# Performance work log

Measured on AMD Instinct MI355X. Metric: run time of the kernel, lower is better.

Reference implementation:

```python
import jax, jax.numpy as jnp
import numpy as np
from jax import lax

D_MODEL = 1024
D_STATE = 128
D_CONV = 4
EXPAND = 2
N_HEADS = 32
CHUNK = 64
D_INNER = EXPAND * D_MODEL                 # 2048
CONV_DIM = D_INNER + 2 * D_STATE           # 2304
D_IN_PROJ = 2 * D_INNER + 2 * D_STATE + N_HEADS  # 4384
HEAD_DIM = D_INNER // N_HEADS              # 64
EPS = 1e-5


def setup_inputs() -> dict:
    key = jax.random.key(0)
    ks = jax.random.split(key, 10)
    u = jax.random.normal(ks[0], (4, 4096, D_MODEL), dtype=jnp.float32)
    in_proj_w = jax.random.normal(ks[1], (D_IN_PROJ, D_MODEL), dtype=jnp.float32) * 0.02
    conv_w = jax.random.normal(ks[2], (CONV_DIM, 1, D_CONV), dtype=jnp.float32) * 0.3
    conv_b = jnp.zeros((CONV_DIM,), dtype=jnp.float32)
    dt_bias = jax.random.uniform(ks[3], (N_HEADS,), minval=-0.5, maxval=0.5, dtype=jnp.float32)
    A_log = jax.random.uniform(ks[4], (N_HEADS,), minval=-0.1, maxval=-0.01, dtype=jnp.float32)
    D = jax.random.uniform(ks[5], (N_HEADS,), minval=0.9, maxval=1.1, dtype=jnp.float32)
    norm_w = jnp.ones((D_INNER,), dtype=jnp.float32)
    out_proj_w = jax.random.normal(ks[6], (D_MODEL, D_INNER), dtype=jnp.float32) * 0.02
    return {"u": u, "in_proj_w": in_proj_w, "conv_w": conv_w, "conv_b": conv_b,
            "dt_bias": dt_bias, "A_log": A_log, "D": D, "norm_w": norm_w,
            "out_proj_w": out_proj_w}


def segsum(x):
    """Stable segment sum. x: (..., T) -> (..., T, T); exp of it is 1-semiseparable."""
    T = x.shape[-1]
    xe = jnp.broadcast_to(x[..., :, None], x.shape + (T,))  # '... d -> ... d e'
    mask_strict = jnp.tril(jnp.ones((T, T), dtype=bool), k=-1)
    xe = jnp.where(mask_strict, xe, 0.0)
    seg = jnp.cumsum(xe, axis=-2)
    mask_incl = jnp.tril(jnp.ones((T, T), dtype=bool), k=0)
    return jnp.where(mask_incl, seg, -jnp.inf)


def ssd(x, A, B, C):
    """x:(b,L,h,p)  A:(b,L,h)  B,C:(b,L,h,n). L multiple of CHUNK."""
    b, Lp, h, p = x.shape
    n = B.shape[-1]
    c = Lp // CHUNK
    x = x.reshape(b, c, CHUNK, h, p)
    A = A.reshape(b, c, CHUNK, h).transpose(0, 3, 1, 2)       # (b,h,c,l)
    B = B.reshape(b, c, CHUNK, h, n)
    C = C.reshape(b, c, CHUNK, h, n)
    A_cumsum = jnp.cumsum(A, axis=-1)                          # (b,h,c,l)
    L = jnp.exp(segsum(A))                                     # (b,h,c,l,l)
    # intra-chunk (diagonal blocks)
    Y_diag = jnp.einsum('bclhn,bcshn,bhcls,bcshp->bclhp', C, B, L, x)
    # chunk-final states
    decay_states = jnp.exp(A_cumsum[:, :, :, -1:] - A_cumsum)  # (b,h,c,l)
    states = jnp.einsum('bclhn,bhcl,bclhp->bchpn', B, decay_states, x)
    init = jnp.zeros_like(states[:, :1])
    states = jnp.concatenate([init, states], axis=1)           # (b,c+1,h,p,n)
    decay_chunk = jnp.exp(segsum(jnp.pad(A_cumsum[:, :, :, -1], ((0, 0), (0, 0), (1, 0)))))
    new_states = jnp.einsum('bhzc,bchpn->bzhpn', decay_chunk, states)
    states, final_state = new_states[:, :-1], new_states[:, -1]
    # inter-chunk (off-diagonal) contribution
    state_decay_out = jnp.exp(A_cumsum)
    Y_off = jnp.einsum('bclhn,bchpn,bhcl->bclhp', C, states, state_decay_out)
    Y = (Y_diag + Y_off).reshape(b, Lp, h, p)
    return Y, final_state


def _forward(u, in_proj_w, conv_w, conv_b, dt_bias, A_log, D, norm_w, out_proj_w):
    b, seq_len, _ = u.shape
    pad = CHUNK - seq_len % CHUNK  # note: full extra chunk when seq_len % CHUNK == 0 (faithful)
    u = jnp.pad(u, ((0, 0), (0, pad), (0, 0)))
    Lp = u.shape[1]
    A = -jnp.exp(A_log)                                        # (h,)
    zxbcdt = jnp.einsum('bld,ed->ble', u, in_proj_w)           # (b,Lp,D_IN_PROJ)
    z = zxbcdt[..., :D_INNER]
    xBC = zxbcdt[..., D_INNER:D_INNER + CONV_DIM]
    dt = zxbcdt[..., -N_HEADS:]
    # causal depthwise conv1d + silu
    xc = xBC.transpose(0, 2, 1)                                # (b,conv_dim,Lp)
    xc = lax.conv_general_dilated(xc, conv_w, window_strides=(1,),
                                  padding=[(D_CONV - 1, 0)],
                                  feature_group_count=CONV_DIM,
                                  dimension_numbers=('NCH', 'OIH', 'NCH'))
    xBC = jax.nn.silu((xc + conv_b[None, :, None]).transpose(0, 2, 1))
    x = xBC[..., :D_INNER].reshape(b, Lp, N_HEADS, HEAD_DIM)
    Bm = xBC[..., D_INNER:D_INNER + D_STATE]
    Cm = xBC[..., D_INNER + D_STATE:]
    Bm = jnp.broadcast_to(Bm[:, :, None, :], (b, Lp, N_HEADS, D_STATE))
    Cm = jnp.broadcast_to(Cm[:, :, None, :], (b, Lp, N_HEADS, D_STATE))
    dt = jax.nn.softplus(dt + dt_bias)                         # (b,Lp,h)
    y, _ = ssd(x * dt[..., None], A * dt, Bm, Cm)
    y = y + x * D[None, None, :, None]
    y = y.reshape(b, Lp, D_INNER)
    # gated RMSNorm
    t = y * jax.nn.silu(z)
    t = t * jax.lax.rsqrt(jnp.mean(t * t, axis=-1, keepdims=True) + EPS) * norm_w
    out = jnp.einsum('bld,ed->ble', t, out_proj_w)
    return out[:, :seq_len]


def reference(u, in_proj_w, conv_w, conv_b, dt_bias, A_log, D, norm_w, out_proj_w):
    return _forward(u, in_proj_w, conv_w, conv_b, dt_bias, A_log, D, norm_w, out_proj_w)
```

## Files before the change

### kernel.cpp

```cpp
#include <hip/hip_runtime.h>
#include <hip/hip_bf16.h>
#include <math.h>


#define BL    16384
#define NCONV 2304
#define LDXP  2336

typedef __hip_bfloat16 bf16;
typedef __attribute__((ext_vector_type(8))) short bf16x8_i;
typedef __attribute__((ext_vector_type(4))) float f32x4;

union BF8 { uint4 u; bf16 h[8]; };
union BF2 { uint u; bf16 h[2]; };

__device__ __forceinline__ void gload_lds16(const void* g, void* l) {
  __builtin_amdgcn_global_load_lds(
      (__attribute__((address_space(1))) void*)(uintptr_t)g,
      (__attribute__((address_space(3))) void*)(uint32_t)(uintptr_t)l,
      16, 0, 0);
}

template<typename TC, bool CLAMPB>
__global__ __launch_bounds__(256) void gemm_bt_mfma(
    const bf16* __restrict__ A, int lda,
    const bf16* __restrict__ B, int ldb,
    TC* __restrict__ C, int ldc, int N, int K)
{
  __shared__ __align__(16) bf16 As[128 * 32];
  __shared__ __align__(16) bf16 Bs[128 * 32];
  const int tid  = threadIdx.x;
  const int lane = tid & 63;
  const int wid  = tid >> 6;

  const int gx  = gridDim.x;
  const int nwg = gx * gridDim.y;
  const int q   = nwg >> 3;
  int id = blockIdx.y * gx + blockIdx.x;
  id = (id & 7) * q + (id >> 3);
  const int bm = (id / gx) * 128;
  const int bn = (id % gx) * 128;

  const int wr = (wid >> 1) * 64;
  const int wc = (wid & 1) * 64;

  f32x4 acc[4][4] = {};

  int aoff[4], boff[4];
  #pragma unroll
  for (int i = 0; i < 4; ++i) {
    aoff[i] = (wr + i * 16 + (lane & 15)) * 32 + (lane >> 4) * 8;
    boff[i] = (wc + i * 16 + (lane & 15)) * 32 + (lane >> 4) * 8;
  }

  const int srow = tid >> 2, scol = (tid & 3) * 8;
  int brow0 = bn + srow, brow1 = bn + 64 + srow;
  if (CLAMPB) { brow0 = min(brow0, N - 1); brow1 = min(brow1, N - 1); }
  const bf16* pA0 = A + (size_t)(bm + srow) * lda + scol;
  const bf16* pA1 = pA0 + (size_t)lda * 64;
  const bf16* pB0 = B + (size_t)brow0 * ldb + scol;
  const bf16* pB1 = B + (size_t)brow1 * ldb + scol;
  bf16* lA0 = As + wid * 512;
  bf16* lA1 = As + 2048 + wid * 512;
  bf16* lB0 = Bs + wid * 512;
  bf16* lB1 = Bs + 2048 + wid * 512;

  for (int k0 = 0; k0 < K; k0 += 32) {
    gload_lds16(pA0, lA0);
    gload_lds16(pA1, lA1);
    gload_lds16(pB0, lB0);
    gload_lds16(pB1, lB1);
    pA0 += 32; pA1 += 32; pB0 += 32; pB1 += 32;
    __syncthreads();
    bf16x8_i af[4], bfr[4];
    #pragma unroll
    for (int i = 0; i < 4; ++i) {
      af[i]  = *(const bf16x8_i*)(As + aoff[i]);
      bfr[i] = *(const bf16x8_i*)(Bs + boff[i]);
    }
    #pragma unroll
    for (int i = 0; i < 4; ++i)
      #pragma unroll
      for (int j = 0; j < 4; ++j)
        acc[i][j] = __builtin_amdgcn_mfma_f32_16x16x32_bf16(
            af[i], bfr[j], acc[i][j], 0, 0, 0);
    __syncthreads();
  }

  const int cr = (lane >> 4) * 4;
  const int cc = lane & 15;
  #pragma unroll
  for (int i = 0; i < 4; ++i) {
    #pragma unroll
    for (int j = 0; j < 4; ++j) {
      const int n = bn + wc + j * 16 + cc;
      if (n < N) {
        #pragma unroll
        for (int r = 0; r < 4; ++r) {
          const int m = bm + wr + i * 16 + cr + r;
          if constexpr (sizeof(TC) == 2)
            ((bf16*)C)[(size_t)m * ldc + n] = __float2bfloat16(acc[i][j][r]);
          else
            ((float*)C)[(size_t)m * ldc + n] = acc[i][j][r];
        }
      }
    }
  }
}

__global__ __launch_bounds__(256) void cvt_f32_bf16(
    const float* __restrict__ in, bf16* __restrict__ out)
{
  const size_t i = (size_t)(blockIdx.x * 256 + threadIdx.x) * 8;
  float4 a = *(const float4*)(in + i);
  float4 b = *(const float4*)(in + i + 4);
  BF8 o;
  o.h[0] = __float2bfloat16(a.x); o.h[1] = __float2bfloat16(a.y);
  o.h[2] = __float2bfloat16(a.z); o.h[3] = __float2bfloat16(a.w);
  o.h[4] = __float2bfloat16(b.x); o.h[5] = __float2bfloat16(b.y);
  o.h[6] = __float2bfloat16(b.z); o.h[7] = __float2bfloat16(b.w);
  *(uint4*)(out + i) = o.u;
}

__global__ __launch_bounds__(256) void dtsp_atot_kernel(
    const bf16* __restrict__ xpre, const float* __restrict__ dt_bias,
    const float* __restrict__ A_log,
    float* __restrict__ dtT, float* __restrict__ Atot)
{
  const int c = blockIdx.x, b = blockIdx.y;
  const int tid = threadIdx.x;
  const int h = tid & 31, lg = tid >> 5;
  __shared__ float red[8][33];
  float s = 0.f, vals[8];
  const bf16* src = xpre + ((size_t)b * 4096 + c * 64 + lg * 8) * LDXP + 2304 + h;
  const float bias = dt_bias[h];
  #pragma unroll
  for (int k = 0; k < 8; ++k) {
    float v = __bfloat162float(src[(size_t)k * LDXP]) + bias;
    v = fmaxf(v, 0.f) + log1pf(expf(-fabsf(v)));
    vals[k] = v; s += v;
  }
  float* dp = dtT + ((size_t)(b * 32 + h)) * 4096 + c * 64 + lg * 8;
  #pragma unroll
  for (int k = 0; k < 8; ++k) dp[k] = vals[k];
  red[lg][h] = s;
  __syncthreads();
  if (tid < 32) {
    float t = 0.f;
    #pragma unroll
    for (int g = 0; g < 8; ++g) t += red[g][tid];
    Atot[((size_t)b * 64 + c) * 32 + tid] = -expf(A_log[tid]) * t;
  }
}

__global__ __launch_bounds__(256) void conv_silu_kernel(
    const bf16* __restrict__ xpre,
    const float* __restrict__ conv_w,
    const float* __restrict__ conv_b,
    bf16* __restrict__ xBC)
{
  const int ch = blockIdx.x * 256 + threadIdx.x;
  const int t0 = blockIdx.y * 8;
  const int bb = blockIdx.z;
  const float w0 = conv_w[ch*4+0], w1 = conv_w[ch*4+1];
  const float w2 = conv_w[ch*4+2], w3 = conv_w[ch*4+3];
  const float bias = conv_b[ch];
  const size_t rb = (size_t)bb * 4096;
  const bf16* src = xpre + ch;
  float v0 = (t0 >= 3) ? __bfloat162float(src[(rb + t0 - 3) * LDXP]) : 0.f;
  float v1 = (t0 >= 2) ? __bfloat162float(src[(rb + t0 - 2) * LDXP]) : 0.f;
  float v2 = (t0 >= 1) ? __bfloat162float(src[(rb + t0 - 1) * LDXP]) : 0.f;
  for (int t = t0; t < t0 + 8; ++t) {
    float v3 = __bfloat162float(src[(rb + t) * LDXP]);
    float o = bias + w0*v0 + w1*v1 + w2*v2 + w3*v3;
    o = o / (1.f + expf(-o));
    xBC[(rb + t) * NCONV + ch] = __float2bfloat16(o);
    v0 = v1; v1 = v2; v2 = v3;
  }
}

__device__ __forceinline__ int swz8(int row) { return ((row >> 3) & 7) << 3; }

__global__ __launch_bounds__(256) void s1_localstate(
    const bf16* __restrict__ xBC, const float* __restrict__ dtT,
    const float* __restrict__ A_log, bf16* __restrict__ states, int b)
{
  const int hh = blockIdx.x, c = blockIdx.y;
  const int tid = threadIdx.x, lane = tid & 63, wid = tid >> 6;
  __shared__ bf16 BT[128 * 72];
  __shared__ bf16 xwT[64 * 72];
  __shared__ bf16 Sout[64 * 136];
  const size_t r0 = (size_t)b * 4096 + (size_t)c * 64;

  BF8 regB[4], regx[2];
  #pragma unroll
  for (int k = 0; k < 4; ++k) {
    int id = tid + k * 256, l = id >> 4, n0 = (id & 15) * 8;
    regB[k].u = *(const uint4*)(xBC + (r0 + l) * NCONV + 2048 + n0);
  }
  #pragma unroll
  for (int k = 0; k < 2; ++k) {
    int id = tid + k * 256, l = id >> 3, p0 = (id & 7) * 8;
    regx[k].u = *(const uint4*)(xBC + (r0 + l) * NCONV + hh * 64 + p0);
  }

  float d = dtT[((size_t)(b * 32 + hh)) * 4096 + c * 64 + lane];
  float Ah = -expf(A_log[hh]);
  float v = Ah * d;
  #pragma unroll
  for (int off = 1; off < 64; off <<= 1) {
    float up = __shfl_up(v, off, 64);
    if (lane >= off) v += up;
  }
  const float At = __shfl(v, 63, 64);
  const float w = d * __expf(At - v);

  #pragma unroll
  for (int k = 0; k < 4; ++k) {
    int id = tid + k * 256, l = id >> 4, n0 = (id & 15) * 8;
    #pragma unroll
    for (int j = 0; j < 8; ++j) {
      int n = n0 + j;
      BT[n * 72 + (l ^ swz8(n))] = regB[k].h[j];
    }
  }
  #pragma unroll
  for (int k = 0; k < 2; ++k) {
    int id = tid + k * 256, l = id >> 3, p0 = (id & 7) * 8;
    float wv = __shfl(w, l, 64);
    #pragma unroll
    for (int j = 0; j < 8; ++j) {
      int p = p0 + j;
      xwT[p * 72 + (l ^ swz8(p))] =
          __float2bfloat16(__bfloat162float(regx[k].h[j]) * wv);
    }
  }
  __syncthreads();

  const int wr = (wid & 1) * 32;
  const int wc = (wid >> 1) * 64;
  f32x4 acc[2][4] = {};
  #pragma unroll
  for (int ks = 0; ks < 2; ++ks) {
    const int k0 = ks * 32 + (lane >> 4) * 8;
    bf16x8_i a[2], bb[4];
    #pragma unroll
    for (int i = 0; i < 2; ++i) {
      int p = wr + i * 16 + (lane & 15);
      a[i] = *(const bf16x8_i*)(xwT + p * 72 + (k0 ^ swz8(p)));
    }
    #pragma unroll
    for (int j = 0; j < 4; ++j) {
      int n = wc + j * 16 + (lane & 15);
      bb[j] = *(const bf16x8_i*)(BT + n * 72 + (k0 ^ swz8(n)));
    }
    #pragma unroll
    for (int i = 0; i < 2; ++i)
      #pragma unroll
      for (int j = 0; j < 4; ++j)
        acc[i][j] = __builtin_amdgcn_mfma_f32_16x16x32_bf16(
            a[i], bb[j], acc[i][j], 0, 0, 0);
  }

  const int cr = (lane >> 4) * 4, cn = lane & 15;
  #pragma unroll
  for (int i = 0; i < 2; ++i)
    #pragma unroll
    for (int j = 0; j < 4; ++j)
      #pragma unroll
      for (int r = 0; r < 4; ++r)
        Sout[(wr + i * 16 + cr + r) * 136 + (wc + j * 16 + cn)] =
            __float2bfloat16(acc[i][j][r]);
  __syncthreads();
  bf16* sb = states + ((size_t)c * 32 + hh) * 8192;
  #pragma unroll
  for (int k = 0; k < 4; ++k) {
    int id = tid + k * 256, p = id >> 4, n0 = (id & 15) * 8;
    *(uint4*)(sb + p * 128 + n0) = *(const uint4*)(Sout + p * 136 + n0);
  }
}

__global__ __launch_bounds__(256) void s2_scan(
    bf16* __restrict__ states, const float* __restrict__ Atot, int b)
{
  const int h  = blockIdx.x >> 4;
  const int p  = ((blockIdx.x & 15) << 2) | (threadIdx.x >> 6);
  const int n0 = (threadIdx.x & 63) * 2;
  __shared__ float ec[64];
  if (threadIdx.x < 64)
    ec[threadIdx.x] = expf(Atot[((size_t)b * 64 + threadIdx.x) * 32 + h]);
  __syncthreads();
  bf16* ptr = states + ((size_t)h * 64 + p) * 128 + n0;
  const size_t cs = (size_t)32 * 8192;
  float ca = 0.f, cb = 0.f;
  BF2 g0, g1, g2, g3, q0, q1, q2, q3;
  g0.u = *(const uint*)(ptr + 0 * cs);
  g1.u = *(const uint*)(ptr + 1 * cs);
  g2.u = *(const uint*)(ptr + 2 * cs);
  g3.u = *(const uint*)(ptr + 3 * cs);
  for (int g = 0; g < 16; ++g) {
    const int c0 = g * 4;
    if (g < 15) {
      q0.u = *(const uint*)(ptr + (c0 + 4) * cs);
      q1.u = *(const uint*)(ptr + (c0 + 5) * cs);
      q2.u = *(const uint*)(ptr + (c0 + 6) * cs);
      q3.u = *(const uint*)(ptr + (c0 + 7) * cs);
    }
    BF2 o0, o1, o2, o3;
    const float e0 = ec[c0], e1 = ec[c0+1], e2 = ec[c0+2], e3 = ec[c0+3];
    o0.h[0] = __float2bfloat16(ca); o0.h[1] = __float2bfloat16(cb);
    ca = fmaf(e0, ca, __bfloat162float(g0.h[0]));
    cb = fmaf(e0, cb, __bfloat162float(g0.h[1]));
    o1.h[0] = __float2bfloat16(ca); o1.h[1] = __float2bfloat16(cb);
    ca = fmaf(e1, ca, __bfloat162float(g1.h[0]));
    cb = fmaf(e1, cb, __bfloat162float(g1.h[1]));
    o2.h[0] = __float2bfloat16(ca); o2.h[1] = __float2bfloat16(cb);
    ca = fmaf(e2, ca, __bfloat162float(g2.h[0]));
    cb = fmaf(e2, cb, __bfloat162float(g2.h[1]));
    o3.h[0] = __float2bfloat16(ca); o3.h[1] = __float2bfloat16(cb);
    ca = fmaf(e3, ca, __bfloat162float(g3.h[0]));
    cb = fmaf(e3, cb, __bfloat162float(g3.h[1]));
    *(uint*)(ptr + (c0 + 0) * cs) = o0.u;
    *(uint*)(ptr + (c0 + 1) * cs) = o1.u;
    *(uint*)(ptr + (c0 + 2) * cs) = o2.u;
    *(uint*)(ptr + (c0 + 3) * cs) = o3.u;
    g0 = q0; g1 = q1; g2 = q2; g3 = q3;
  }
}

__global__ __launch_bounds__(256) void s3_output(
    const bf16* __restrict__ xBC, const float* __restrict__ dtT,
    const float* __restrict__ A_log, const float* __restrict__ Dp,
    const bf16* __restrict__ states, bf16* __restrict__ Y, int b)
{
  const int hh = blockIdx.x, c = blockIdx.y;
  const int tid = threadIdx.x, lane = tid & 63, wid = tid >> 6;
  __shared__ bf16 Cc[64 * 136];
  __shared__ bf16 Bc[64 * 136];
  __shared__ bf16 Sin[64 * 136];
  __shared__ bf16 xT[64 * 72];
  __shared__ bf16 scb[64 * 72];
  __shared__ float Ac[64], dts[64];
  const size_t r0 = (size_t)b * 4096 + (size_t)c * 64;

  if (tid < 64) {
    float d = dtT[((size_t)(b * 32 + hh)) * 4096 + c * 64 + tid];
    float Ah = -expf(A_log[hh]);
    float v = Ah * d;
    #pragma unroll
    for (int off = 1; off < 64; off <<= 1) {
      float up = __shfl_up(v, off, 64);
      if (tid >= off) v += up;
    }
    Ac[tid] = v; dts[tid] = d;
  }

  #pragma unroll
  for (int k = 0; k < 4; ++k) {
    int id = tid + k * 256, l = id >> 4, n0 = (id & 15) * 8;
    BF8 bv; bv.u = *(const uint4*)(xBC + (r0 + l) * NCONV + 2048 + n0);
    BF8 cv; cv.u = *(const uint4*)(xBC + (r0 + l) * NCONV + 2176 + n0);
    *(uint4*)(Bc + l * 136 + n0) = bv.u;
    *(uint4*)(Cc + l * 136 + n0) = cv.u;
  }
  const bf16* sb = states + ((size_t)c * 32 + hh) * 8192;
  #pragma unroll
  for (int k = 0; k < 4; ++k) {
    int id = tid + k * 256, p = id >> 4, n0 = (id & 15) * 8;
    *(uint4*)(Sin + p * 136 + n0) = *(const uint4*)(sb + p * 128 + n0);
  }
  #pragma unroll
  for (int k = 0; k < 2; ++k) {
    int id = tid + k * 256, l = id >> 3, p0 = (id & 7) * 8;
    BF8 v; v.u = *(const uint4*)(xBC + (r0 + l) * NCONV + hh * 64 + p0);
    #pragma unroll
    for (int j = 0; j < 8; ++j) {
      int p = p0 + j;
      xT[p * 72 + (l ^ swz8(p))] = v.h[j];
    }
  }
  __syncthreads();

  const int wr  = (wid & 1) * 32;
  const int wcs = (wid >> 1) * 32;
  f32x4 as[2][2] = {};
  bf16x8_i afrag[2][4];
  #pragma unroll
  for (int ks = 0; ks < 4; ++ks) {
    const int k0 = ks * 32 + (lane >> 4) * 8;
    #pragma unroll
    for (int i = 0; i < 2; ++i)
      afrag[i][ks] =
          *(const bf16x8_i*)(Cc + (wr + i * 16 + (lane & 15)) * 136 + k0);
    #pragma unroll
    for (int j = 0; j < 2; ++j) {
      bf16x8_i bfr =
          *(const bf16x8_i*)(Bc + (wcs + j * 16 + (lane & 15)) * 136 + k0);
      #pragma unroll
      for (int i = 0; i < 2; ++i)
        as[i][j] = __builtin_amdgcn_mfma_f32_16x16x32_bf16(
            afrag[i][ks], bfr, as[i][j], 0, 0, 0);
    }
  }
  const int cr = (lane >> 4) * 4, cc = lane & 15;
  #pragma unroll
  for (int i = 0; i < 2; ++i) {
    #pragma unroll
    for (int r = 0; r < 4; ++r) {
      const int l = wr + i * 16 + cr + r;
      const float acl = Ac[l];
      #pragma unroll
      for (int j = 0; j < 2; ++j) {
        const int s = wcs + j * 16 + cc;
        float val = (s <= l) ? as[i][j][r] * __expf(acl - Ac[s]) * dts[s] : 0.f;
        scb[l * 72 + s] = __float2bfloat16(val);
      }
    }
  }
  __syncthreads();

  f32x4 ay[2][2] = {};
  #pragma unroll
  for (int ks = 0; ks < 4; ++ks) {
    const int k0 = ks * 32 + (lane >> 4) * 8;
    #pragma unroll
    for (int j = 0; j < 2; ++j) {
      bf16x8_i bfr =
          *(const bf16x8_i*)(Sin + (wcs + j * 16 + (lane & 15)) * 136 + k0);
      #pragma unroll
      for (int i = 0; i < 2; ++i)
        ay[i][j] = __builtin_amdgcn_mfma_f32_16x16x32_bf16(
            afrag[i][ks], bfr, ay[i][j], 0, 0, 0);
    }
  }
  #pragma unroll
  for (int i = 0; i < 2; ++i)
    #pragma unroll
    for (int r = 0; r < 4; ++r) {
      const float dk = __expf(Ac[wr + i * 16 + cr + r]);
      #pragma unroll
      for (int j = 0; j < 2; ++j) ay[i][j][r] *= dk;
    }
  #pragma unroll
  for (int ks = 0; ks < 2; ++ks) {
    const int k0 = ks * 32 + (lane >> 4) * 8;
    bf16x8_i a2[2], b2[2];
    #pragma unroll
    for (int i = 0; i < 2; ++i)
      a2[i] = *(const bf16x8_i*)(scb + (wr + i * 16 + (lane & 15)) * 72 + k0);
    #pragma unroll
    for (int j = 0; j < 2; ++j) {
      int p = wcs + j * 16 + (lane & 15);
      b2[j] = *(const bf16x8_i*)(xT + p * 72 + (k0 ^ swz8(p)));
    }
    #pragma unroll
    for (int i = 0; i < 2; ++i)
      #pragma unroll
      for (int j = 0; j < 2; ++j)
        ay[i][j] = __builtin_amdgcn_mfma_f32_16x16x32_bf16(
            a2[i], b2[j], ay[i][j], 0, 0, 0);
  }
  const float Dh = Dp[hh];
  bf16* Yb = Bc;
  #pragma unroll
  for (int i = 0; i < 2; ++i)
    #pragma unroll
    for (int r = 0; r < 4; ++r) {
      const int l = wr + i * 16 + cr + r;
      #pragma unroll
      for (int j = 0; j < 2; ++j) {
        const int p = wcs + j * 16 + cc;
        float xv = __bfloat162float(xT[p * 72 + (l ^ swz8(p))]);
        Yb[l * 136 + p] = __float2bfloat16(ay[i][j][r] + Dh * xv);
      }
    }
  __syncthreads();
  #pragma unroll
  for (int k = 0; k < 2; ++k) {
    int id = tid + k * 256, l = id >> 3, p0 = (id & 7) * 8;
    *(uint4*)(Y + (r0 + l) * 2048 + hh * 64 + p0) =
        *(const uint4*)(Yb + l * 136 + p0);
  }
}

__global__ __launch_bounds__(256) void gate_rmsnorm_kernel(
    bf16* __restrict__ y, const bf16* __restrict__ z,
    const float* __restrict__ norm_w)
{
  const size_t row = blockIdx.x;
  const int tid = threadIdx.x;
  __shared__ float red[4];
  const bf16* zr = z + row * 2048;
  bf16* yr = y + row * 2048;
  BF8 zv, yv;
  zv.u = *(const uint4*)(zr + tid * 8);
  yv.u = *(const uint4*)(yr + tid * 8);
  float t[8];
  float local = 0.f;
  #pragma unroll
  for (int j = 0; j < 8; ++j) {
    float zz = __bfloat162float(zv.h[j]);
    float yy = __bfloat162float(yv.h[j]);
    float tv = yy * (zz / (1.f + expf(-zz)));
    t[j] = tv;
    local += tv * tv;
  }
  #pragma unroll
  for (int off = 32; off; off >>= 1) local += __shfl_down(local, off, 64);
  if ((tid & 63) == 0) red[tid >> 6] = local;
  __syncthreads();
  const float total = red[0] + red[1] + red[2] + red[3];
  const float scale = rsqrtf(total * (1.f / 2048.f) + 1e-5f);
  BF8 o;
  #pragma unroll
  for (int j = 0; j < 8; ++j)
    o.h[j] = __float2bfloat16(t[j] * scale * norm_w[tid * 8 + j]);
  *(uint4*)(yr + tid * 8) = o.u;
}

extern "C" void kernel_launch(void* const* d_in, const int* in_sizes, int n_in,
                              void* d_out, int out_size, void* d_ws, size_t ws_size,
                              hipStream_t stream) {
  (void)in_sizes; (void)n_in; (void)out_size; (void)ws_size;
  const float* u          = (const float*)d_in[0];
  const float* in_proj_w  = (const float*)d_in[1];
  const float* conv_w     = (const float*)d_in[2];
  const float* conv_b     = (const float*)d_in[3];
  const float* dt_bias    = (const float*)d_in[4];
  const float* A_log      = (const float*)d_in[5];
  const float* Dp         = (const float*)d_in[6];
  const float* norm_w     = (const float*)d_in[7];
  const float* out_proj_w = (const float*)d_in[8];
  float* out = (float*)d_out;

  char* ws = (char*)d_ws;
  bf16*  u_bf   = (bf16*)ws;
  bf16*  xpre   = (bf16*)(ws + 33554432);
  bf16*  xBCc   = (bf16*)(ws + 110100480);
  float* dtT    = (float*)(ws + 185597952);
  bf16*  W_xpre = (bf16*)(ws + 187695104);
  bf16*  W_z    = (bf16*)(ws + 192479232);
  bf16*  w_out  = (bf16*)(ws + 196673536);
  float* Atot   = (float*)(ws + 200867840);
  bf16*  states = (bf16*)(ws + 200900608);
  bf16*  ybuf   = xpre;
  bf16*  zbuf   = xBCc;

  cvt_f32_bf16<<<dim3(8192), 256, 0, stream>>>(u, u_bf);
  cvt_f32_bf16<<<dim3(1168), 256, 0, stream>>>(in_proj_w + (size_t)2048*1024,
                                               W_xpre);
  cvt_f32_bf16<<<dim3(1024), 256, 0, stream>>>(in_proj_w, W_z);
  cvt_f32_bf16<<<dim3(1024), 256, 0, stream>>>(out_proj_w, w_out);
  gemm_bt_mfma<bf16, true><<<dim3(19, 128), 256, 0, stream>>>(
      u_bf, 1024, W_xpre, 1024, xpre, LDXP, 2336, 1024);
  dtsp_atot_kernel<<<dim3(64, 4), 256, 0, stream>>>(xpre, dt_bias, A_log,
                                                    dtT, Atot);
  conv_silu_kernel<<<dim3(9, 512, 4), 256, 0, stream>>>(xpre, conv_w, conv_b,
                                                        xBCc);
  for (int b = 0; b < 4; ++b) {
    s1_localstate<<<dim3(32, 64), 256, 0, stream>>>(xBCc, dtT, A_log,
                                                    states, b);
    s2_scan<<<dim3(512), 256, 0, stream>>>(states, Atot, b);
    s3_output<<<dim3(32, 64), 256, 0, stream>>>(xBCc, dtT, A_log, Dp,
                                                states, ybuf, b);
  }
  gemm_bt_mfma<bf16, false><<<dim3(16, 128), 256, 0, stream>>>(
      u_bf, 1024, W_z, 1024, zbuf, 2048, 2048, 1024);
  gate_rmsnorm_kernel<<<dim3(BL), 256, 0, stream>>>(ybuf, zbuf, norm_w);
  gemm_bt_mfma<float, false><<<dim3(8, 128), 256, 0, stream>>>(
      ybuf, 2048, w_out, 2048, out, 1024, 1024, 2048);
}
```

Baseline: 602.3 us.

## Double-buffer GEMM LDS tiles with BK=64, XOR swizzle and async prefetch

Rewrites the bf16 MFMA GEMM main loop to use two LDS buffers with a K-tile of 64. The next tile is prefetched with global_load_lds while the current one is consumed, with manual vmcnt waits and raw s_barrier in place of two __syncthreads per step. It also adds an XOR swizzle on LDS column offsets to reduce bank conflicts and raises wave priority around the MFMA block. LDS use grows to 64 KB per block, which may reduce occupancy, and K must now be a multiple of 64.

```diff
diff --git a/kernel.cpp b/kernel.cpp
--- a/kernel.cpp
+++ b/kernel.cpp
@@ -27,8 +27,8 @@
     const bf16* __restrict__ B, int ldb,
     TC* __restrict__ C, int ldc, int N, int K)
 {
-  __shared__ __align__(16) bf16 As[128 * 32];
-  __shared__ __align__(16) bf16 Bs[128 * 32];
+  __shared__ __align__(16) bf16 As2[2][128 * 64];
+  __shared__ __align__(16) bf16 Bs2[2][128 * 64];
   const int tid  = threadIdx.x;
   const int lane = tid & 63;
   const int wid  = tid >> 6;
@@ -46,45 +46,80 @@
 
   f32x4 acc[4][4] = {};
 
-  int aoff[4], boff[4];
+  int aoff[4][2], boff[4][2];
   #pragma unroll
   for (int i = 0; i < 4; ++i) {
-    aoff[i] = (wr + i * 16 + (lane & 15)) * 32 + (lane >> 4) * 8;
-    boff[i] = (wc + i * 16 + (lane & 15)) * 32 + (lane >> 4) * 8;
-  }
-
-  const int srow = tid >> 2, scol = (tid & 3) * 8;
-  int brow0 = bn + srow, brow1 = bn + 64 + srow;
-  if (CLAMPB) { brow0 = min(brow0, N - 1); brow1 = min(brow1, N - 1); }
-  const bf16* pA0 = A + (size_t)(bm + srow) * lda + scol;
-  const bf16* pA1 = pA0 + (size_t)lda * 64;
-  const bf16* pB0 = B + (size_t)brow0 * ldb + scol;
-  const bf16* pB1 = B + (size_t)brow1 * ldb + scol;
-  bf16* lA0 = As + wid * 512;
-  bf16* lA1 = As + 2048 + wid * 512;
-  bf16* lB0 = Bs + wid * 512;
-  bf16* lB1 = Bs + 2048 + wid * 512;
-
-  for (int k0 = 0; k0 < K; k0 += 32) {
-    gload_lds16(pA0, lA0);
-    gload_lds16(pA1, lA1);
-    gload_lds16(pB0, lB0);
-    gload_lds16(pB1, lB1);
-    pA0 += 32; pA1 += 32; pB0 += 32; pB1 += 32;
-    __syncthreads();
-    bf16x8_i af[4], bfr[4];
-    #pragma unroll
-    for (int i = 0; i < 4; ++i) {
-      af[i]  = *(const bf16x8_i*)(As + aoff[i]);
-      bfr[i] = *(const bf16x8_i*)(Bs + boff[i]);
-    }
-    #pragma unroll
-    for (int i = 0; i < 4; ++i)
-      #pragma unroll
-      for (int j = 0; j < 4; ++j)
-        acc[i][j] = __builtin_amdgcn_mfma_f32_16x16x32_bf16(
-            af[i], bfr[j], acc[i][j], 0, 0, 0);
-    __syncthreads();
+    const int ar = wr + i * 16 + (lane & 15);
+    const int br = wc + i * 16 + (lane & 15);
+    const int asw = ((ar >> 2) & 3) << 4;
+    const int bsw = ((br >> 2) & 3) << 4;
+    #pragma unroll
+    for (int ks = 0; ks < 2; ++ks) {
+      const int c0 = ks * 32 + (lane >> 4) * 8;
+      aoff[i][ks] = ar * 64 + (c0 ^ asw);
+      boff[i][ks] = br * 64 + (c0 ^ bsw);
+    }
+  }
+
+  const int srow = tid >> 3;
+  const int sj   = tid & 7;
+  const bf16* pA[4];
+  const bf16* pB[4];
+  #pragma unroll
+  for (int i = 0; i < 4; ++i) {
+    const int r  = i * 32 + srow;
+    const int js = sj ^ (((r >> 2) & 3) << 1);
+    int brow = bn + r;
+    if (CLAMPB) brow = min(brow, N - 1);
+    pA[i] = A + (size_t)(bm + r) * lda + js * 8;
+    pB[i] = B + (size_t)brow * ldb + js * 8;
+  }
+
+  const int NT = K >> 6;
+  #pragma unroll
+  for (int i = 0; i < 4; ++i) {
+    gload_lds16(pA[i], &As2[0][0] + i * 2048 + wid * 512);
+    gload_lds16(pB[i], &Bs2[0][0] + i * 2048 + wid * 512);
+    pA[i] += 64; pB[i] += 64;
+  }
+
+  for (int t = 0; t < NT; ++t) {
+    const int cur = t & 1;
+    if (t + 1 < NT) {
+      bf16* dA = &As2[cur ^ 1][0];
+      bf16* dB = &Bs2[cur ^ 1][0];
+      #pragma unroll
+      for (int i = 0; i < 4; ++i) {
+        gload_lds16(pA[i], dA + i * 2048 + wid * 512);
+        gload_lds16(pB[i], dB + i * 2048 + wid * 512);
+        pA[i] += 64; pB[i] += 64;
+      }
+      asm volatile("s_waitcnt vmcnt(8)" ::: "memory");
+    } else {
+      asm volatile("s_waitcnt vmcnt(0)" ::: "memory");
+    }
+    __builtin_amdgcn_sched_barrier(0);
+    __builtin_amdgcn_s_barrier();
+    const bf16* Ab = &As2[cur][0];
+    const bf16* Bb = &Bs2[cur][0];
+    __builtin_amdgcn_s_setprio(1);
+    #pragma unroll
+    for (int ks = 0; ks < 2; ++ks) {
+      bf16x8_i af[4], bfr[4];
+      #pragma unroll
+      for (int i = 0; i < 4; ++i) {
+        af[i]  = *(const bf16x8_i*)(Ab + aoff[i][ks]);
+        bfr[i] = *(const bf16x8_i*)(Bb + boff[i][ks]);
+      }
+      #pragma unroll
+      for (int i = 0; i < 4; ++i)
+        #pragma unroll
+        for (int j = 0; j < 4; ++j)
+          acc[i][j] = __builtin_amdgcn_mfma_f32_16x16x32_bf16(
+              af[i], bfr[j], acc[i][j], 0, 0, 0);
+    }
+    __builtin_amdgcn_s_setprio(0);
+    __builtin_amdgcn_s_barrier();
   }
 
   const int cr = (lane >> 4) * 4;
```

After: 516.6 us. -14.2%, faster.
